# Optimization experiments

Hardware: AMD Instinct MI355X
Metric: run time of the kernel (lower is better)

The kernel has to match this reference:

```python
import jax, jax.numpy as jnp
import numpy as np

T = 100000


def setup_inputs() -> dict:
    key = jax.random.key(0)
    u = jax.random.normal(key, (1, T, 2), dtype=jnp.float32)
    M = jnp.array([20.0, 10.0], dtype=jnp.float32)
    C = jnp.array([10.0, 10.0, 10.0], dtype=jnp.float32)   # trainable damping
    K = jnp.array([2000.0, 1000.0, 5000.0], dtype=jnp.float32)
    x0 = jnp.zeros((1, 4), dtype=jnp.float32)              # [y1, v1, y2, v2]
    dt = jnp.asarray(0.002, dtype=jnp.float32)
    return {"u": u, "M": M, "C": C, "K": K, "x0": x0, "dt": dt}


def reference(u, M, C, K, x0, dt):
    # 2x2 coupled damping / stiffness matrices (same math as _fun)
    Cm = jnp.stack([jnp.stack([C[0] + C[1], -C[1]]),
                    jnp.stack([-C[1], C[2] + C[1]])])
    Km = jnp.stack([jnp.stack([K[0] + K[1], -K[1]]),
                    jnp.stack([-K[1], K[2] + K[1]])])

    def accel(z, v, ut):  # z, v, ut: [2]
        return (ut - Cm @ v - Km @ z) / M

    def step(carry, ut):
        y, v = carry
        k1 = accel(y, v, ut)
        y2 = y + v * (dt / 2.0); v2 = v + k1 * (dt / 2.0)
        k2 = accel(y2, v2, ut)
        y3 = y + v2 * (dt / 2.0); v3 = v + k2 * (dt / 2.0)
        k3 = accel(y3, v3, ut)
        y4 = y + v3 * dt; v4 = v + k3 * dt
        k4 = accel(y4, v4, ut)
        yn = y + (dt / 6.0) * (v + 2.0 * v2 + 2.0 * v3 + v4)
        vn = v + (dt / 6.0) * (k1 + 2.0 * k2 + 2.0 * k3 + k4)
        return (yn, vn), yn

    y0 = x0[0, ::2]   # positions [y1, y2]
    v0 = x0[0, 1::2]  # velocities [v1, v2]
    _, ys = jax.lax.scan(step, (y0, v0), u[0])  # ys: [T, 2]
    return ys[None]  # [1, T, 2] position sequence, matching RNN output y
```

## Files before the change

### kernel.cpp

```cpp
#include <hip/hip_runtime.h>


#define LSTEP  16
#define TPB    256
#define MAXNB  256

__device__ inline void accel_d(const double* M, const double* Cm, const double* Km,
                               const double* u, const double* z, const double* v, double* a) {
  a[0] = (u[0] - Cm[0] * v[0] - Cm[1] * v[1] - Km[0] * z[0] - Km[1] * z[1]) / M[0];
  a[1] = (u[1] - Cm[2] * v[0] - Cm[3] * v[1] - Km[2] * z[0] - Km[3] * z[1]) / M[1];
}

__device__ inline void rk4_step_d(const double* M, const double* Cm, const double* Km,
                                  double dt, double* y, double* v, const double* u) {
  double k1[2], k2[2], k3[2], k4[2];
  double y2[2], v2[2], y3[2], v3[2], y4[2], v4[2];
  double h = dt * 0.5;
  accel_d(M, Cm, Km, u, y, v, k1);
  y2[0] = y[0] + v[0] * h;  y2[1] = y[1] + v[1] * h;
  v2[0] = v[0] + k1[0] * h; v2[1] = v[1] + k1[1] * h;
  accel_d(M, Cm, Km, u, y2, v2, k2);
  y3[0] = y[0] + v2[0] * h;  y3[1] = y[1] + v2[1] * h;
  v3[0] = v[0] + k2[0] * h;  v3[1] = v[1] + k2[1] * h;
  accel_d(M, Cm, Km, u, y3, v3, k3);
  y4[0] = y[0] + v3[0] * dt; y4[1] = y[1] + v3[1] * dt;
  v4[0] = v[0] + k3[0] * dt; v4[1] = v[1] + k3[1] * dt;
  accel_d(M, Cm, Km, u, y4, v4, k4);
  double s = dt / 6.0;
  double yn0 = y[0] + s * (v[0] + 2.0 * v2[0] + 2.0 * v3[0] + v4[0]);
  double yn1 = y[1] + s * (v[1] + 2.0 * v2[1] + 2.0 * v3[1] + v4[1]);
  double vn0 = v[0] + s * (k1[0] + 2.0 * k2[0] + 2.0 * k3[0] + k4[0]);
  double vn1 = v[1] + s * (k1[1] + 2.0 * k2[1] + 2.0 * k3[1] + k4[1]);
  y[0] = yn0; y[1] = yn1; v[0] = vn0; v[1] = vn1;
}

__device__ inline void build_cols(const float* Mp, const float* Cp, const float* Kp,
                                  const float* dtp, float* Af, float* Bf, double* Ad) {
  int tid = threadIdx.x;
  if (tid < 6) {
    double M[2]  = {(double)Mp[0], (double)Mp[1]};
    double Cm[4] = {(double)Cp[0] + (double)Cp[1], -(double)Cp[1],
                    -(double)Cp[1], (double)Cp[2] + (double)Cp[1]};
    double Km[4] = {(double)Kp[0] + (double)Kp[1], -(double)Kp[1],
                    -(double)Kp[1], (double)Kp[2] + (double)Kp[1]};
    double dt = (double)dtp[0];
    double y[2] = {0, 0}, v[2] = {0, 0}, u[2] = {0, 0};
    if      (tid == 0) y[0] = 1.0;
    else if (tid == 1) y[1] = 1.0;
    else if (tid == 2) v[0] = 1.0;
    else if (tid == 3) v[1] = 1.0;
    else if (tid == 4) u[0] = 1.0;
    else               u[1] = 1.0;
    rk4_step_d(M, Cm, Km, dt, y, v, u);
    if (tid < 4) {
      Af[0 * 4 + tid] = (float)y[0]; Af[1 * 4 + tid] = (float)y[1];
      Af[2 * 4 + tid] = (float)v[0]; Af[3 * 4 + tid] = (float)v[1];
      Ad[0 * 4 + tid] = y[0]; Ad[1 * 4 + tid] = y[1];
      Ad[2 * 4 + tid] = v[0]; Ad[3 * 4 + tid] = v[1];
    } else {
      int j = tid - 4;
      Bf[0 * 2 + j] = (float)y[0]; Bf[1 * 2 + j] = (float)y[1];
      Bf[2 * 2 + j] = (float)v[0]; Bf[3 * 2 + j] = (float)v[1];
    }
  }
}

__device__ inline float4 mv4(const float* A, float4 x) {
  float4 r;
  r.x = A[0]  * x.x + A[1]  * x.y + A[2]  * x.z + A[3]  * x.w;
  r.y = A[4]  * x.x + A[5]  * x.y + A[6]  * x.z + A[7]  * x.w;
  r.z = A[8]  * x.x + A[9]  * x.y + A[10] * x.z + A[11] * x.w;
  r.w = A[12] * x.x + A[13] * x.y + A[14] * x.z + A[15] * x.w;
  return r;
}
__device__ inline float4 f4add(float4 a, float4 b) {
  return make_float4(a.x + b.x, a.y + b.y, a.z + b.z, a.w + b.w);
}
__device__ inline float4 stepf(const float* a, const float* b, float4 s, float2 ut) {
  float4 r;
  r.x = a[0]  * s.x + a[1]  * s.y + a[2]  * s.z + a[3]  * s.w + b[0] * ut.x + b[1] * ut.y;
  r.y = a[4]  * s.x + a[5]  * s.y + a[6]  * s.z + a[7]  * s.w + b[2] * ut.x + b[3] * ut.y;
  r.z = a[8]  * s.x + a[9]  * s.y + a[10] * s.z + a[11] * s.w + b[4] * ut.x + b[5] * ut.y;
  r.w = a[12] * s.x + a[13] * s.y + a[14] * s.z + a[15] * s.w + b[6] * ut.x + b[7] * ut.y;
  return r;
}
__device__ inline void mm4(const float* X, const float* Y, float* Z) {
#pragma unroll
  for (int i = 0; i < 4; ++i)
#pragma unroll
    for (int j = 0; j < 4; ++j)
      Z[i * 4 + j] = X[i * 4 + 0] * Y[0 * 4 + j] + X[i * 4 + 1] * Y[1 * 4 + j]
                   + X[i * 4 + 2] * Y[2 * 4 + j] + X[i * 4 + 3] * Y[3 * 4 + j];
}

__device__ inline double matmul16(double a, double b, int i, int j) {
  double acc = 0.0;
#pragma unroll
  for (int k = 0; k < 4; ++k)
    acc += __shfl(a, i * 4 + k) * __shfl(b, k * 4 + j);
  return acc;
}

__global__ __launch_bounds__(TPB) void kFused(
    const float* __restrict__ u, const float* M, const float* C, const float* K,
    const float* dtp, const float* x0, int T,
    float4* __restrict__ agg, int* __restrict__ flags, float2* __restrict__ out) {
  __shared__ float  Af[16], Bf[8];
  __shared__ double Ad[16];
  __shared__ float  Tt[256][16];
  __shared__ float  Wt[32][16];
  __shared__ float4 S[TPB];
  __shared__ float4 sBsh;

  int tid = threadIdx.x;
  int b   = blockIdx.x;

  int j  = b * TPB + tid;
  int t0 = j * LSTEP;
  bool full = (t0 + LSTEP <= T);
  float4 uu[LSTEP / 2];
  if (full) {
    const float4* u4 = (const float4*)(u + 2 * t0);
#pragma unroll
    for (int i = 0; i < LSTEP / 2; ++i) uu[i] = u4[i];
  }

  build_cols(M, C, K, dtp, Af, Bf, Ad);
  if (tid == 0) {
#pragma unroll
    for (int e = 0; e < 16; ++e) {
      float v = ((e >> 2) == (e & 3)) ? 1.f : 0.f;
      Tt[0][e] = v; Wt[0][e] = v;
    }
  }
  __syncthreads();

  if (tid < 16) {
    int i = tid >> 2, jj = tid & 3;
    double m = Ad[tid];
#pragma unroll
    for (int lvl = 1; lvl <= 16; ++lvl) {
      m = matmul16(m, m, i, jj);
      if (lvl >= 4 && lvl <= 11) Tt[1 << (lvl - 4)][tid] = (float)m;
      if (lvl >= 12)             Wt[1 << (lvl - 12)][tid] = (float)m;
    }
  }
  __syncthreads();

#pragma unroll
  for (int d = 1; d < 8; ++d) {
    int off = 1 << d;
    if (tid > off && tid < 2 * off)
      mm4(&Tt[tid - off][0], &Tt[off][0], &Tt[tid][0]);
    if (d <= 4) {
      int k = tid - 128;
      if (k > off && k < 2 * off && k < 25 && tid >= 128 + off + 1)
        mm4(&Wt[k - off][0], &Wt[off][0], &Wt[k][0]);
    }
    __syncthreads();
  }

  float a[16], bb[8];
#pragma unroll
  for (int e = 0; e < 16; ++e) a[e] = Af[e];
#pragma unroll
  for (int e = 0; e < 8; ++e) bb[e] = Bf[e];

  float4 c = make_float4(0.f, 0.f, 0.f, 0.f);
  if (full) {
#pragma unroll
    for (int i = 0; i < LSTEP / 2; ++i) {
      c = stepf(a, bb, c, make_float2(uu[i].x, uu[i].y));
      c = stepf(a, bb, c, make_float2(uu[i].z, uu[i].w));
    }
  } else {
    const float2* u2 = (const float2*)u;
    for (int i = 0; i < LSTEP; ++i) {
      int t = t0 + i;
      if (t >= T) break;
      c = stepf(a, bb, c, u2[t]);
    }
  }

  S[tid] = c;
  __syncthreads();
#pragma unroll
  for (int k = 0; k < 8; ++k) {
    int off = 1 << k;
    float4 add = make_float4(0.f, 0.f, 0.f, 0.f);
    bool act = (tid >= off);
    if (act) add = mv4(&Tt[off][0], S[tid - off]);
    __syncthreads();
    if (act) S[tid] = f4add(S[tid], add);
    __syncthreads();
  }
  float4 E = (tid == 0) ? make_float4(0.f, 0.f, 0.f, 0.f) : S[tid - 1];

  float4 s0v = make_float4(x0[0], x0[2], x0[1], x0[3]);
  if (tid == 0) {
    float4 o = S[TPB - 1];
    if (b == 0) o = f4add(mv4(&Wt[1][0], s0v), o);
    agg[b] = o;
    __threadfence();
    __hip_atomic_store(&flags[b], 1, __ATOMIC_RELEASE, __HIP_MEMORY_SCOPE_AGENT);
  }
  float4 sB;
  if (b == 0) {
    sB = s0v;
  } else {
    if (tid < 64) {
      float4 acc = make_float4(0.f, 0.f, 0.f, 0.f);
      if (tid < b) {
        int p = tid;
        while (__hip_atomic_load(&flags[p], __ATOMIC_ACQUIRE, __HIP_MEMORY_SCOPE_AGENT) != 1) {}
        acc = mv4(&Wt[b - 1 - p][0], agg[p]);
      }
#pragma unroll
      for (int o2 = 32; o2 >= 1; o2 >>= 1) {
        acc.x += __shfl_xor(acc.x, o2);
        acc.y += __shfl_xor(acc.y, o2);
        acc.z += __shfl_xor(acc.z, o2);
        acc.w += __shfl_xor(acc.w, o2);
      }
      if (tid == 0) sBsh = acc;
    }
    __syncthreads();
    sB = sBsh;
  }

  float4 st = f4add(mv4(&Tt[tid][0], sB), E);

  if (full) {
    float4* o4 = (float4*)(out + t0);
#pragma unroll
    for (int i = 0; i < LSTEP / 2; ++i) {
      st = stepf(a, bb, st, make_float2(uu[i].x, uu[i].y));
      float2 ya = make_float2(st.x, st.y);
      st = stepf(a, bb, st, make_float2(uu[i].z, uu[i].w));
      o4[i] = make_float4(ya.x, ya.y, st.x, st.y);
    }
  } else {
    const float2* u2 = (const float2*)u;
    for (int i = 0; i < LSTEP; ++i) {
      int t = t0 + i;
      if (t >= T) break;
      st = stepf(a, bb, st, u2[t]);
      out[t] = make_float2(st.x, st.y);
    }
  }
}

__global__ void kSerialAll(const float* u, const float* Mp, const float* Cp, const float* Kp,
                           const float* dtp, const float* x0, int T, float2* out) {
  if (threadIdx.x != 0 || blockIdx.x != 0) return;
  double M[2]  = {(double)Mp[0], (double)Mp[1]};
  double Cm[4] = {(double)Cp[0] + (double)Cp[1], -(double)Cp[1],
                  -(double)Cp[1], (double)Cp[2] + (double)Cp[1]};
  double Km[4] = {(double)Kp[0] + (double)Kp[1], -(double)Kp[1],
                  -(double)Kp[1], (double)Kp[2] + (double)Kp[1]};
  double dt = (double)dtp[0];
  double y[2] = {(double)x0[0], (double)x0[2]};
  double v[2] = {(double)x0[1], (double)x0[3]};
  for (int t = 0; t < T; ++t) {
    double uu[2] = {(double)u[2 * t], (double)u[2 * t + 1]};
    rk4_step_d(M, Cm, Km, dt, y, v, uu);
    out[t] = make_float2((float)y[0], (float)y[1]);
  }
}

extern "C" void kernel_launch(void* const* d_in, const int* in_sizes, int n_in,
                              void* d_out, int out_size, void* d_ws, size_t ws_size,
                              hipStream_t stream) {
  (void)n_in; (void)out_size;
  const float* u   = (const float*)d_in[0];
  const float* M   = (const float*)d_in[1];
  const float* C   = (const float*)d_in[2];
  const float* K   = (const float*)d_in[3];
  const float* x0  = (const float*)d_in[4];
  const float* dt  = (const float*)d_in[5];
  int T = in_sizes[0] / 2;
  float2* out = (float2*)d_out;

  int nch = (T + LSTEP - 1) / LSTEP;
  int nb  = (nch + TPB - 1) / TPB;
  size_t need = (size_t)MAXNB * (sizeof(float4) + sizeof(int));
  if (nb > 64 || ws_size < need) {
    kSerialAll<<<1, 64, 0, stream>>>(u, M, C, K, dt, x0, T, out);
    return;
  }
  float4* agg  = (float4*)d_ws;
  int* flags   = (int*)(agg + MAXNB);
  kFused<<<nb, TPB, 0, stream>>>(u, M, C, K, dt, x0, T, agg, flags, out);
}
```

Baseline: 75.73 us.

## Split fused decoupled-lookback scan into separate scan and emit kernels

The single fused kernel, where blocks spin-wait on global flags for earlier blocks' aggregates, is replaced by two launches. The first computes per-chunk local states, exclusive prefixes and block aggregates, and block 0 writes the transition tables to workspace. The second reads them back, combines the prior block aggregates with the initial state, and re-runs the recurrence to emit outputs. This removes the inter-block spin synchronisation and its dependence on all blocks being co-resident, at the cost of an extra launch and global round trips for the prefixes and tables.

```diff
diff --git a/kernel.cpp b/kernel.cpp
--- a/kernel.cpp
+++ b/kernel.cpp
@@ -3,7 +3,7 @@
 
 #define LSTEP  16
 #define TPB    256
-#define MAXNB  256
+#define MAXNB  64
 
 __device__ inline void accel_d(const double* M, const double* Cm, const double* Km,
                                const double* u, const double* z, const double* v, double* a) {
@@ -101,16 +101,17 @@
   return acc;
 }
 
-__global__ __launch_bounds__(TPB) void kFused(
+__global__ __launch_bounds__(TPB) void kScan(
     const float* __restrict__ u, const float* M, const float* C, const float* K,
-    const float* dtp, const float* x0, int T,
-    float4* __restrict__ agg, int* __restrict__ flags, float2* __restrict__ out) {
+    const float* dtp, int T,
+    float4* __restrict__ agg, float4* __restrict__ Ebuf,
+    float* __restrict__ TabT, float* __restrict__ TabW,
+    float* __restrict__ TabA, float* __restrict__ TabB) {
   __shared__ float  Af[16], Bf[8];
   __shared__ double Ad[16];
-  __shared__ float  Tt[256][16];
-  __shared__ float  Wt[32][16];
+  __shared__ __align__(16) float Tt[256][16];
+  __shared__ __align__(16) float Wt[64][16];
   __shared__ float4 S[TPB];
-  __shared__ float4 sBsh;
 
   int tid = threadIdx.x;
   int b   = blockIdx.x;
@@ -139,7 +140,7 @@
     int i = tid >> 2, jj = tid & 3;
     double m = Ad[tid];
 #pragma unroll
-    for (int lvl = 1; lvl <= 16; ++lvl) {
+    for (int lvl = 1; lvl <= 17; ++lvl) {
       m = matmul16(m, m, i, jj);
       if (lvl >= 4 && lvl <= 11) Tt[1 << (lvl - 4)][tid] = (float)m;
       if (lvl >= 12)             Wt[1 << (lvl - 12)][tid] = (float)m;
@@ -152,9 +153,9 @@
     int off = 1 << d;
     if (tid > off && tid < 2 * off)
       mm4(&Tt[tid - off][0], &Tt[off][0], &Tt[tid][0]);
-    if (d <= 4) {
+    if (d <= 5 && tid >= 128) {
       int k = tid - 128;
-      if (k > off && k < 2 * off && k < 25 && tid >= 128 + off + 1)
+      if (k > off && k < 2 * off && k < 64)
         mm4(&Wt[k - off][0], &Wt[off][0], &Wt[k][0]);
     }
     __syncthreads();
@@ -194,41 +195,82 @@
     if (act) S[tid] = f4add(S[tid], add);
     __syncthreads();
   }
-  float4 E = (tid == 0) ? make_float4(0.f, 0.f, 0.f, 0.f) : S[tid - 1];
+
+  Ebuf[j] = (tid == 0) ? make_float4(0.f, 0.f, 0.f, 0.f) : S[tid - 1];
+  if (tid == TPB - 1) agg[b] = S[tid];
+  if (b == 0) {
+    float4*       dstT = (float4*)(TabT + tid * 16);
+    const float4* srcT = (const float4*)&Tt[tid][0];
+#pragma unroll
+    for (int e = 0; e < 4; ++e) dstT[e] = srcT[e];
+    if (tid < 64) {
+      float4*       dstW = (float4*)(TabW + tid * 16);
+      const float4* srcW = (const float4*)&Wt[tid][0];
+#pragma unroll
+      for (int e = 0; e < 4; ++e) dstW[e] = srcW[e];
+    }
+    if (tid < 16) TabA[tid] = Af[tid];
+    if (tid < 8)  TabB[tid] = Bf[tid];
+  }
+}
+
+__global__ __launch_bounds__(TPB) void kEmit(
+    const float* __restrict__ u, const float* __restrict__ x0, int T,
+    const float4* __restrict__ agg, const float4* __restrict__ Ebuf,
+    const float* __restrict__ TabT, const float* __restrict__ TabW,
+    const float* __restrict__ TabA, const float* __restrict__ TabB,
+    float2* __restrict__ out) {
+  __shared__ float  Afs[16], Bfs[8];
+  __shared__ float4 sBsh;
+
+  int tid = threadIdx.x;
+  int b   = blockIdx.x;
+  int j   = b * TPB + tid;
+  int t0  = j * LSTEP;
+  bool full = (t0 + LSTEP <= T);
+
+  float4 uu[LSTEP / 2];
+  if (full) {
+    const float4* u4 = (const float4*)(u + 2 * t0);
+#pragma unroll
+    for (int i = 0; i < LSTEP / 2; ++i) uu[i] = u4[i];
+  }
+
+  const float4* tr = (const float4*)(TabT + tid * 16);
+  float4 T0 = tr[0], T1 = tr[1], T2 = tr[2], T3 = tr[3];
+  float4 E  = Ebuf[j];
+
+  if (tid < 16)       Afs[tid] = TabA[tid];
+  else if (tid < 24)  Bfs[tid - 16] = TabB[tid - 16];
 
   float4 s0v = make_float4(x0[0], x0[2], x0[1], x0[3]);
-  if (tid == 0) {
-    float4 o = S[TPB - 1];
-    if (b == 0) o = f4add(mv4(&Wt[1][0], s0v), o);
-    agg[b] = o;
-    __threadfence();
-    __hip_atomic_store(&flags[b], 1, __ATOMIC_RELEASE, __HIP_MEMORY_SCOPE_AGENT);
-  }
-  float4 sB;
-  if (b == 0) {
-    sB = s0v;
-  } else {
-    if (tid < 64) {
-      float4 acc = make_float4(0.f, 0.f, 0.f, 0.f);
-      if (tid < b) {
-        int p = tid;
-        while (__hip_atomic_load(&flags[p], __ATOMIC_ACQUIRE, __HIP_MEMORY_SCOPE_AGENT) != 1) {}
-        acc = mv4(&Wt[b - 1 - p][0], agg[p]);
-      }
-#pragma unroll
-      for (int o2 = 32; o2 >= 1; o2 >>= 1) {
-        acc.x += __shfl_xor(acc.x, o2);
-        acc.y += __shfl_xor(acc.y, o2);
-        acc.z += __shfl_xor(acc.z, o2);
-        acc.w += __shfl_xor(acc.w, o2);
-      }
-      if (tid == 0) sBsh = acc;
-    }
-    __syncthreads();
-    sB = sBsh;
-  }
-
-  float4 st = f4add(mv4(&Tt[tid][0], sB), E);
+  if (tid < 64) {
+    float4 acc = make_float4(0.f, 0.f, 0.f, 0.f);
+    if (tid < b)        acc = mv4(TabW + (size_t)(b - 1 - tid) * 16, agg[tid]);
+    else if (tid == b)  acc = mv4(TabW + (size_t)b * 16, s0v);
+#pragma unroll
+    for (int o2 = 32; o2 >= 1; o2 >>= 1) {
+      acc.x += __shfl_xor(acc.x, o2);
+      acc.y += __shfl_xor(acc.y, o2);
+      acc.z += __shfl_xor(acc.z, o2);
+      acc.w += __shfl_xor(acc.w, o2);
+    }
+    if (tid == 0) sBsh = acc;
+  }
+  __syncthreads();
+  float4 sB = sBsh;
+
+  float4 st;
+  st.x = T0.x * sB.x + T0.y * sB.y + T0.z * sB.z + T0.w * sB.w + E.x;
+  st.y = T1.x * sB.x + T1.y * sB.y + T1.z * sB.z + T1.w * sB.w + E.y;
+  st.z = T2.x * sB.x + T2.y * sB.y + T2.z * sB.z + T2.w * sB.w + E.z;
+  st.w = T3.x * sB.x + T3.y * sB.y + T3.z * sB.z + T3.w * sB.w + E.w;
+
+  float a[16], bb[8];
+#pragma unroll
+  for (int e = 0; e < 16; ++e) a[e] = Afs[e];
+#pragma unroll
+  for (int e = 0; e < 8; ++e) bb[e] = Bfs[e];
 
   if (full) {
     float4* o4 = (float4*)(out + t0);
@@ -283,12 +325,21 @@
 
   int nch = (T + LSTEP - 1) / LSTEP;
   int nb  = (nch + TPB - 1) / TPB;
-  size_t need = (size_t)MAXNB * (sizeof(float4) + sizeof(int));
-  if (nb > 64 || ws_size < need) {
+
+  size_t need = sizeof(float4) * MAXNB
+              + sizeof(float4) * (size_t)MAXNB * TPB
+              + sizeof(float) * (256 * 16 + 64 * 16 + 16 + 8);
+  if (nb > MAXNB || ws_size < need) {
     kSerialAll<<<1, 64, 0, stream>>>(u, M, C, K, dt, x0, T, out);
     return;
   }
   float4* agg  = (float4*)d_ws;
-  int* flags   = (int*)(agg + MAXNB);
-  kFused<<<nb, TPB, 0, stream>>>(u, M, C, K, dt, x0, T, agg, flags, out);
-}
+  float4* Ebuf = agg + MAXNB;
+  float*  TabT = (float*)(Ebuf + (size_t)MAXNB * TPB);
+  float*  TabW = TabT + 256 * 16;
+  float*  TabA = TabW + 64 * 16;
+  float*  TabB = TabA + 16;
+
+  kScan<<<nb, TPB, 0, stream>>>(u, M, C, K, dt, T, agg, Ebuf, TabT, TabW, TabA, TabB);
+  kEmit<<<nb, TPB, 0, stream>>>(u, x0, T, agg, Ebuf, TabT, TabW, TabA, TabB, out);
+}
```

Measured after the change: 76.80 us. About the same (+1.4%).
